# Optimization experiments

Measured on AMD Instinct MI355X. Metric: run time of the kernel, lower is better.

## Reference

```python
import jax, jax.numpy as jnp
import numpy as np

B, C, L, H, P, NF = 32, 512, 336, 1024, 192, 4  # batch, enc_in, seq_len, nflow_dim, pred_len, nflow_layers


def setup_inputs() -> dict:
    key = jax.random.key(0)
    ks = jax.random.split(key, 18)
    s = 0.02  # small init so exp(0.5*sigma) stays tame
    f32 = jnp.float32
    return {
        "x_enc": jax.random.normal(ks[0], (B, C, L), f32),
        "eps": jax.random.normal(ks[1], (B, C, P), f32),
        # GRU params (torch gate order r,z,n)
        "gru_wih": jax.random.normal(ks[2], (3 * H, C), f32) * s,
        "gru_whh": jax.random.normal(ks[3], (3 * H, H), f32) * s,
        "gru_bih": jax.random.normal(ks[4], (3 * H,), f32) * s,
        "gru_bhh": jax.random.normal(ks[5], (3 * H,), f32) * s,
        # enc_fix: Linear(1, enc_in)
        "encfix_w": jax.random.normal(ks[6], (C, 1), f32) * s,
        "encfix_b": jax.random.normal(ks[7], (C,), f32) * s,
        # distribution_enc_mu / presigma: Linear(d_ff, pred_len)
        "encmu_w": jax.random.normal(ks[8], (P, H), f32) * s,
        "encmu_b": jax.random.normal(ks[9], (P,), f32) * s,
        "encps_w": jax.random.normal(ks[10], (P, H), f32) * s,
        "encps_b": jax.random.normal(ks[11], (P,), f32) * s,
        # flow layers (stacked): Conv1d(C,C,2), Linear(H+P,P) x2
        "conv_w": jax.random.normal(ks[12], (NF, C, C, 2), f32) * s,
        "conv_b": jax.random.normal(ks[13], (NF, C), f32) * s,
        "mu_w": jax.random.normal(ks[14], (NF, P, H + P), f32) * s,
        "mu_b": jax.random.normal(ks[15], (NF, P), f32) * s,
        "sg_w": jax.random.normal(ks[16], (NF, P, H + P), f32) * s,
        "sg_b": jax.random.normal(ks[17], (NF, P), f32) * s,
    }


def reference(x_enc, eps, gru_wih, gru_whh, gru_bih, gru_bhh,
              encfix_w, encfix_b, encmu_w, encmu_b, encps_w, encps_b,
              conv_w, conv_b, mu_w, mu_b, sg_w, sg_b):
    h_dim = gru_whh.shape[1]
    pred_len = encmu_w.shape[0]
    x = jnp.transpose(x_enc, (0, 2, 1))            # (B, L, C)
    xw = x @ gru_wih.T + gru_bih                   # (B, L, 3H) input projections, precomputed

    def step(h, g):
        gh = h @ gru_whh.T + gru_bhh
        ir, iz, in_ = jnp.split(g, 3, axis=-1)
        hr, hz, hn = jnp.split(gh, 3, axis=-1)
        r = jax.nn.sigmoid(ir + hr)
        z = jax.nn.sigmoid(iz + hz)
        n = jnp.tanh(in_ + r * hn)
        return (1.0 - z) * n + z * h, None

    h0 = jnp.zeros((x.shape[0], h_dim), x.dtype)
    hT, _ = jax.lax.scan(step, h0, jnp.swapaxes(xw, 0, 1))  # (B, H) final hidden

    # enc_fix: Linear(1, enc_in) applied on last axis of (B, H, 1)
    enc = hT[:, :, None] * encfix_w[:, 0] + encfix_b        # (B, H, C)
    enc = jnp.transpose(enc, (0, 2, 1))                      # (B, C, H)

    enc_mu = enc @ encmu_w.T + encmu_b                       # (B, C, P)
    enc_sigma = jax.nn.softplus(enc @ encps_w.T + encps_b)   # (B, C, P)
    sample = enc_mu + jnp.exp(0.5 * enc_sigma) * eps         # (B, C, P)
    h = jnp.concatenate([enc, sample], axis=2)               # (B, C, H+P)

    for l in range(conv_w.shape[0]):
        w = conv_w[l]                                        # (C, C, 2)
        # Conv1d kernel size 2, valid padding, then ReLU
        hc = (jnp.einsum('bit,oi->bot', h[:, :, :-1], w[:, :, 0])
              + jnp.einsum('bit,oi->bot', h[:, :, 1:], w[:, :, 1])
              + conv_b[l][:, None])
        hc = jax.nn.relu(hc)
        hc = jnp.concatenate([hc[:, :, :1], hc], axis=2)     # re-pad to (B, C, H+P)
        mu = hc @ mu_w[l].T + mu_b[l]                        # (B, C, P)
        sg = hc @ sg_w[l].T + sg_b[l]                        # (B, C, P)
        sample = mu + jnp.exp(0.5 * sg) * sample * 0.1
        h = h + 0.1 * jnp.concatenate([hc[:, :, :hc.shape[2] - pred_len], sample], axis=2)

    return jnp.transpose(sample, (0, 2, 1))                  # (B, P, C)
```

## Files before the change

### kernel.cpp

```cpp
#include <hip/hip_runtime.h>

using u16 = unsigned short;
using u32 = unsigned int;
using u64 = unsigned long long;
using f32x4 = __attribute__((ext_vector_type(4))) float;
using s16x8 = __attribute__((ext_vector_type(8))) short;
using u32x4 = __attribute__((ext_vector_type(4))) unsigned int;

__device__ __forceinline__ u16 f2b(float f) {
  union { float f; u32 u; } v; v.f = f;
  u32 r = v.u + 0x7fffu + ((v.u >> 16) & 1u);
  return (u16)(r >> 16);
}
__device__ __forceinline__ float b2f(u16 h) {
  union { u32 u; float f; } v; v.u = ((u32)h) << 16; return v.f;
}
__device__ __forceinline__ void gl_lds16(const u16* g, u16* l) {
  __builtin_amdgcn_global_load_lds(
      (const __attribute__((address_space(1))) void*)g,
      (__attribute__((address_space(3))) void*)l, 16, 0, 0);
}
__device__ __forceinline__ float fsigm(float x) {
  return 1.f / (1.f + __expf(-x));
}
__device__ __forceinline__ float ftanh(float x) {
  float ax = fabsf(x);
  float e2 = __expf(2.f * ax);
  float th = 1.f - 2.f / (e2 + 1.f);
  return copysignf(th, x);
}

__global__ void k_cast(const float* __restrict__ s, u16* __restrict__ d, int n) {
  int i = blockIdx.x * 256 + threadIdx.x;
  if (i < n) d[i] = f2b(s[i]);
}

__global__ void k_musgw(const float* __restrict__ muw, const float* __restrict__ sgw,
                        u16* __restrict__ dst, int n) {
  int i = blockIdx.x * 256 + threadIdx.x;
  if (i >= n) return;
  int l = i / (384 * 1216);
  int r = (i / 1216) % 384;
  int k = i % 1216;
  int p = r >> 1;
  const float* s = (r & 1) ? (sgw + ((long)l * 192 + p) * 1216 + k)
                           : (muw + ((long)l * 192 + p) * 1216 + k);
  dst[i] = f2b(*s);
}

__global__ void k_catb(const float* __restrict__ mub, const float* __restrict__ sgb,
                       float* __restrict__ catb) {
  int i = blockIdx.x * 256 + threadIdx.x;
  if (i >= 1536) return;
  int l = i / 384, r = i % 384;
  int p = r >> 1;
  catb[i] = (r & 1) ? sgb[l * 192 + p] : mub[l * 192 + p];
}

__global__ void k_convw(const float* __restrict__ cw, u16* __restrict__ Aw, int n) {
  int i = blockIdx.x * 256 + threadIdx.x;
  if (i >= n) return;
  int l = i >> 19;
  int r1 = i & 524287;
  int o = r1 >> 10;
  int r2 = r1 & 1023;
  int tap = r2 >> 9;
  int ii = r2 & 511;
  Aw[i] = f2b(cw[(((long)(l * 512 + o)) * 512 + ii) * 2 + tap]);
}

__global__ void k_gruw(const float* __restrict__ whh, u16* __restrict__ blob) {
  int i = blockIdx.x * 256 + threadIdx.x;
  int lane = i & 63;
  int c = (i >> 6) & 15;
  int g = (i >> 10) % 3;
  int wwv = i / 3072;
  int wv = wwv & 3, wg = wwv >> 2;
  int jbw = wv & 1, kw = wv >> 1;
  int j = wg * 32 + jbw * 16 + (lane & 15);
  int k = kw * 512 + c * 32 + (lane >> 4) * 8;
  const float* src = whh + ((long)(g * 1024 + j)) * 1024 + k;
  u16* dst = blob + (long)i * 8;
#pragma unroll
  for (int v = 0; v < 8; ++v) dst[v] = f2b(src[v]);
}

__global__ __launch_bounds__(256) void k_txe(const float* __restrict__ x, u16* __restrict__ xT) {
  __shared__ float tile[32][33];
  int l0 = blockIdx.x * 32, c0 = blockIdx.y * 32, b = blockIdx.z;
  int tid = threadIdx.x;
  for (int q = 0; q < 4; ++q) {
    int idx = tid + q * 256;
    int r = idx >> 5, cc = idx & 31;
    int l = l0 + cc;
    tile[r][cc] = (l < 336) ? x[((long)b * 512 + c0 + r) * 336 + l] : 0.f;
  }
  __syncthreads();
  for (int q = 0; q < 4; ++q) {
    int idx = tid + q * 256;
    int r = idx >> 5, cc = idx & 31;
    int l = l0 + r;
    if (l < 336) xT[((long)b * 336 + l) * 512 + c0 + cc] = f2b(tile[cc][r]);
  }
}

__global__ __launch_bounds__(256) void k_hbt(const float* __restrict__ hbuf, u16* __restrict__ hbT) {
  __shared__ float tile[32][65];
  int t0 = blockIdx.x * 64, c0 = blockIdx.y * 32, b = blockIdx.z;
  int tid = threadIdx.x;
#pragma unroll
  for (int q = 0; q < 2; ++q) {
    int idx = tid + q * 256;
    int r = idx >> 4, col = (idx & 15) * 4;
    *(float4*)&tile[r][col] =
        *(const float4*)&hbuf[((long)b * 512 + c0 + r) * 1216 + t0 + col];
  }
  __syncthreads();
#pragma unroll
  for (int q = 0; q < 2; ++q) {
    int idx = tid + q * 256;
    int t = idx >> 3, cg = (idx & 7) * 4;
    ushort4 o;
    o.x = f2b(tile[cg + 0][t]);
    o.y = f2b(tile[cg + 1][t]);
    o.z = f2b(tile[cg + 2][t]);
    o.w = f2b(tile[cg + 3][t]);
    *(ushort4*)&hbT[((long)b * 1216 + t0 + t) * 512 + c0 + cg] = o;
  }
}

__global__ __launch_bounds__(256) void k_out(const float* __restrict__ smp, float* __restrict__ out) {
  __shared__ float tile[32][33];
  int p0 = blockIdx.x * 32, c0 = blockIdx.y * 32, b = blockIdx.z;
  int tid = threadIdx.x;
  for (int q = 0; q < 4; ++q) {
    int idx = tid + q * 256;
    int r = idx >> 5, cc = idx & 31;
    tile[r][cc] = smp[((long)b * 512 + c0 + r) * 192 + p0 + cc];
  }
  __syncthreads();
  for (int q = 0; q < 4; ++q) {
    int idx = tid + q * 256;
    int r = idx >> 5, cc = idx & 31;
    out[((long)b * 192 + p0 + r) * 512 + c0 + cc] = tile[cc][r];
  }
}

template<int MODE>
__global__ __launch_bounds__(256, 2)
void gemm_bt(const u16* __restrict__ A, const u16* __restrict__ Bt,
             void* __restrict__ Cv, const float* __restrict__ bias,
             int M, int N, int K, int lda, int ldb, int ldc,
             long sA, long sB, long sC,
             int arowmax, int browmax, int NT,
             float* __restrict__ hbufp, long sH,
             float* __restrict__ sampleP, long sS)
{
  __shared__ u16 As[128 * 64];
  __shared__ u16 Bs[128 * 64];
  const int tid = threadIdx.x;
  const int lane = tid & 63;
  const int wv = tid >> 6;
  const int z = blockIdx.z;
  const u16* Ab = A + (long)z * sA;
  const u16* Bb = Bt + (long)z * sB;
  const int m0 = blockIdx.y * 128, n0 = blockIdx.x * 128;
  const int wm = (wv >> 1) * 64, wn = (wv & 1) * 64;

  f32x4 acc[4][4] = {};

  for (int kt = 0; kt < K; kt += 64) {
#pragma unroll
    for (int s = 0; s < 4; ++s) {
      int row = (wv * 4 + s) * 8 + (lane >> 3);
      int ck = (lane & 7) ^ (row & 7);
      int ra = m0 + row; if (ra > arowmax) ra = arowmax;
      gl_lds16(Ab + (long)ra * lda + (kt + ck * 8), As + (wv * 4 + s) * 512);
      int rb = n0 + row; if (rb > browmax) rb = browmax;
      gl_lds16(Bb + (long)rb * ldb + (kt + ck * 8), Bs + (wv * 4 + s) * 512);
    }
    __syncthreads();
#pragma unroll
    for (int kk = 0; kk < 64; kk += 32) {
      s16x8 af[4], bfr[4];
#pragma unroll
      for (int i = 0; i < 4; ++i) {
        int rowa = wm + i * 16 + (lane & 15);
        int offa = (rowa * 128 + (kk + 8 * (lane >> 4)) * 2) ^ ((rowa & 7) << 4);
        af[i] = *(const s16x8*)((const char*)As + offa);
        int rowb = wn + i * 16 + (lane & 15);
        int offb = (rowb * 128 + (kk + 8 * (lane >> 4)) * 2) ^ ((rowb & 7) << 4);
        bfr[i] = *(const s16x8*)((const char*)Bs + offb);
      }
#pragma unroll
      for (int i = 0; i < 4; ++i)
#pragma unroll
        for (int j = 0; j < 4; ++j)
          acc[i][j] = __builtin_amdgcn_mfma_f32_16x16x32_bf16(af[i], bfr[j], acc[i][j], 0, 0, 0);
    }
    __syncthreads();
  }

  u16* Cb16 = (u16*)Cv;
#pragma unroll
  for (int i = 0; i < 4; ++i) {
#pragma unroll
    for (int j = 0; j < 4; ++j) {
      const int mb = m0 + wm + i * 16 + 4 * (lane >> 4);
      const int n = n0 + wn + j * 16 + (lane & 15);
      if (n >= NT) continue;
      f32x4 v = acc[i][j];
      if (MODE == 0) {
        float bn = bias[n];
        u16* Cp = Cb16;
#pragma unroll
        for (int r = 0; r < 4; ++r)
          Cp[(long)(mb + r) * ldc + n] = f2b(v[r] + bn);
      } else if (MODE == 4) {
        float bn = bias[n];
        u16* Cp = Cb16;
#pragma unroll
        for (int r = 0; r < 4; ++r) {
          int m = mb + r;
          int bb = m / 336;
          int tt = m - bb * 336;
          Cp[(long)(tt * 32 + bb) * ldc + n] = f2b(v[r] + bn);
        }
      } else if (MODE == 2) {
        u16* Cp = Cb16 + (long)z * sC;
        float* hb = hbufp + (long)z * sH;
#pragma unroll
        for (int r = 0; r < 4; ++r) {
          int m = mb + r;
          float x = v[r] + bias[m];
          x = fmaxf(x, 0.0f);
          u16 hx = f2b(x);
          Cp[(long)m * ldc + (n + 1)] = hx;
          if (n + 1 < 1024) hb[(long)m * 1216 + (n + 1)] += 0.1f * x;
          if (n == 0) { Cp[(long)m * ldc] = hx; hb[(long)m * 1216] += 0.1f * x; }
        }
      } else {
        float bn = bias[n];
        float* hb = hbufp + (long)z * sH;
        float* smp = sampleP + (long)z * sS;
        const int p = n >> 1;
#pragma unroll
        for (int r = 0; r < 4; ++r) {
          float val = v[r] + bn;
          float other = __shfl_xor(val, 1);
          if ((lane & 1) == 0) {
            int m = mb + r;
            long si = (long)m * 192 + p;
            float snew = val + __expf(0.5f * other) * smp[si] * 0.1f;
            smp[si] = snew;
            hb[(long)m * 1216 + 1024 + p] += 0.1f * snew;
          }
        }
      }
    }
  }
}

__global__ __launch_bounds__(256, 1)
void k_gru(const u16* __restrict__ xw, const u16* __restrict__ wblob,
           const float* __restrict__ bhh, u64* __restrict__ hfA, u64* __restrict__ hfB,
           float* __restrict__ hTt, float* __restrict__ hTn, u32* __restrict__ flags)
{
  __shared__ float part[6][32][32];
  const int tid = threadIdx.x;
  const int lane = tid & 63;
  const int wv = tid >> 6;
  const int wg = blockIdx.x;
  const int jbw = wv & 1, kw = wv >> 1;

  s16x8 bfr[3][16];
  {
    const u16* wp = wblob + (long)(wg * 4 + wv) * 24576 + lane * 8;
#pragma unroll
    for (int g = 0; g < 3; ++g)
#pragma unroll
      for (int c = 0; c < 16; ++c)
        bfr[g][c] = *(const s16x8*)(wp + (g * 16 + c) * 512);
  }

  const int bq = tid & 31, jg = tid >> 5;
  const int j0 = wg * 32 + jg * 4;
  float b3[3][4];
#pragma unroll
  for (int g = 0; g < 3; ++g)
#pragma unroll
    for (int jj = 0; jj < 4; ++jj) b3[g][jj] = bhh[g * 1024 + j0 + jj];
  ushort4 hold = make_ushort4(0, 0, 0, 0);

  const long hoff64 = ((long)(wg * 2 + (bq >> 4)) * 64 + (bq & 15) + 16 * (jg >> 1)) * 2 + (jg & 1);
  const int myflag = wg * 32;

  for (int t = 0; t < 336; ++t) {
    const u64* __restrict__ hr = (t & 1) ? hfB : hfA;
    u64* __restrict__ hw = (t & 1) ? hfA : hfB;

    const u16* xp = xw + ((long)t * 32 + bq) * 3072 + j0;
    ushort4 xr = *(const ushort4*)(xp);
    ushort4 xz = *(const ushort4*)(xp + 1024);
    ushort4 xn = *(const ushort4*)(xp + 2048);

    if (t > 0) {
      if (wv == 0) {
        const int fi = (lane & 31) * 32;
        int spins = 0;
        while (true) {
          u32 v = __hip_atomic_load(&flags[fi], __ATOMIC_RELAXED, __HIP_MEMORY_SCOPE_AGENT);
          if (__ballot(v >= (u32)t) == ~0ull) break;
          __builtin_amdgcn_s_sleep(1);
          if (++spins > (1 << 22)) break;
        }
      }
    }
    __syncthreads();
    __builtin_amdgcn_sched_barrier(0);

    u32x4 md[32];
#pragma unroll
    for (int c = 0; c < 16; ++c) {
      const int cg = kw * 16 + c;
      u64 a0 = (u64)(const void*)(hr + ((long)(cg * 2 + 0) * 64 + lane) * 2);
      u64 a1 = (u64)(const void*)(hr + ((long)(cg * 2 + 1) * 64 + lane) * 2);
      asm volatile("global_load_dwordx4 %0, %1, off sc1" : "=v"(md[2 * c]) : "v"(a0) : "memory");
      asm volatile("global_load_dwordx4 %0, %1, off sc1" : "=v"(md[2 * c + 1]) : "v"(a1) : "memory");
    }
    asm volatile("s_waitcnt vmcnt(0)" ::: "memory");
    __builtin_amdgcn_sched_barrier(0);

    f32x4 acc[2][3] = {};
#pragma unroll
    for (int c = 0; c < 16; ++c) {
      union { u32x4 d; s16x8 v; } a0u, a1u;
      a0u.d = md[2 * c]; a1u.d = md[2 * c + 1];
#pragma unroll
      for (int g = 0; g < 3; ++g) {
        acc[0][g] = __builtin_amdgcn_mfma_f32_16x16x32_bf16(a0u.v, bfr[g][c], acc[0][g], 0, 0, 0);
        acc[1][g] = __builtin_amdgcn_mfma_f32_16x16x32_bf16(a1u.v, bfr[g][c], acc[1][g], 0, 0, 0);
      }
    }
    {
      const int jl = jbw * 16 + (lane & 15);
      const int swz = ((jl & 1) << 4) | ((jl & 6) << 1);
      const int s4 = (lane >> 4) * 4;
#pragma unroll
      for (int p = 0; p < 2; ++p)
#pragma unroll
        for (int g = 0; g < 3; ++g)
          *(f32x4*)&part[kw * 3 + g][jl][(16 * p + s4) ^ swz] = acc[p][g];
    }
    __syncthreads();

    float hnew[4];
#pragma unroll
    for (int jj = 0; jj < 4; ++jj) {
      const int jl = jg * 4 + jj;
      const int swz = ((jl & 1) << 4) | ((jl & 6) << 1);
      const int slot = bq ^ swz;
      float s0 = part[0][jl][slot] + part[3][jl][slot] + b3[0][jj];
      float s1 = part[1][jl][slot] + part[4][jl][slot] + b3[1][jj];
      float s2 = part[2][jl][slot] + part[5][jl][slot] + b3[2][jj];
      float xrv = b2f(((const u16*)&xr)[jj]);
      float xzv = b2f(((const u16*)&xz)[jj]);
      float xnv = b2f(((const u16*)&xn)[jj]);
      float rg = fsigm(xrv + s0);
      float zg = fsigm(xzv + s1);
      float ng = ftanh(xnv + rg * s2);
      float holdv = b2f(((const u16*)&hold)[jj]);
      hnew[jj] = (1.f - zg) * ng + zg * holdv;
    }
    ((u16*)&hold)[0] = f2b(hnew[0]);
    ((u16*)&hold)[1] = f2b(hnew[1]);
    ((u16*)&hold)[2] = f2b(hnew[2]);
    ((u16*)&hold)[3] = f2b(hnew[3]);

    {
      union { ushort4 s; u32 d[2]; } hq; hq.s = hold;
      u32 p0 = (u32)__shfl_xor((int)hq.d[0], 32);
      u32 p1 = (u32)__shfl_xor((int)hq.d[1], 32);
      if ((lane & 32) == 0) {
        union { u32 d[4]; u32x4 v; } st;
        st.d[0] = hq.d[0]; st.d[1] = hq.d[1]; st.d[2] = p0; st.d[3] = p1;
        u64 ad = (u64)(void*)(hw + hoff64);
        asm volatile("global_store_dwordx4 %0, %1, off sc1" :: "v"(ad), "v"(st.v) : "memory");
      }
    }
    if (t == 335) {
#pragma unroll
      for (int jj = 0; jj < 4; ++jj) hTt[(j0 + jj) * 32 + bq] = hnew[jj];
      *(float4*)(hTn + bq * 1024 + j0) = make_float4(hnew[0], hnew[1], hnew[2], hnew[3]);
    }
    asm volatile("s_waitcnt vmcnt(0)" ::: "memory");
    __syncthreads();
    if (tid == 0)
      __hip_atomic_store(&flags[myflag], (u32)(t + 1), __ATOMIC_RELAXED, __HIP_MEMORY_SCOPE_AGENT);
  }
}

__global__ __launch_bounds__(256) void k_encsmall(
    const float* __restrict__ hTt, const float* __restrict__ emw, const float* __restrict__ epw,
    float* __restrict__ Am, float* __restrict__ Asg, float* __restrict__ Sm, float* __restrict__ Ssg)
{
  int q = blockIdx.x * 256 + threadIdx.x;
  int p = q >> 3, bg = q & 7;
  float am[4] = {0.f, 0.f, 0.f, 0.f}, as[4] = {0.f, 0.f, 0.f, 0.f};
  float sm = 0.f, ss = 0.f;
  const float* wmp = emw + (long)p * 1024;
  const float* wsp = epw + (long)p * 1024;
  for (int k = 0; k < 1024; ++k) {
    float a = wmp[k], b = wsp[k];
    f32x4 hv = *(const f32x4*)(hTt + k * 32 + bg * 4);
#pragma unroll
    for (int i = 0; i < 4; ++i) { am[i] += a * hv[i]; as[i] += b * hv[i]; }
    sm += a; ss += b;
  }
#pragma unroll
  for (int i = 0; i < 4; ++i) {
    Am[(bg * 4 + i) * 192 + p] = am[i];
    Asg[(bg * 4 + i) * 192 + p] = as[i];
  }
  if (bg == 0) { Sm[p] = sm; Ssg[p] = ss; }
}

__global__ __launch_bounds__(256) void k_build(
    const float* __restrict__ hTn, const float* __restrict__ fw, const float* __restrict__ fb,
    const float* __restrict__ Am, const float* __restrict__ Asg,
    const float* __restrict__ Sm, const float* __restrict__ Ssg,
    const float* __restrict__ emub, const float* __restrict__ epsb,
    const float* __restrict__ eps, float* __restrict__ hbuf, float* __restrict__ sample)
{
  int c = blockIdx.x, b = blockIdx.y, tid = threadIdx.x;
  float fwc = fw[c], fbc = fb[c];
  long hb0 = ((long)b * 512 + c) * 1216;
  const float* hrow = hTn + b * 1024;
  for (int q = 0; q < 4; ++q) {
    int tt = tid + q * 256;
    hbuf[hb0 + tt] = hrow[tt] * fwc + fbc;
  }
  if (tid < 192) {
    int p = tid;
    float mu_e = fwc * Am[b * 192 + p] + fbc * Sm[p] + emub[p];
    float pse = fwc * Asg[b * 192 + p] + fbc * Ssg[p] + epsb[p];
    float sgv = (pse > 15.f) ? pse : log1pf(__expf(pse));
    long si = ((long)b * 512 + c) * 192 + p;
    float smp = mu_e + __expf(0.5f * sgv) * eps[si];
    sample[si] = smp;
    hbuf[hb0 + 1024 + p] = smp;
  }
}

extern "C" void kernel_launch(void* const* d_in, const int* in_sizes, int n_in,
                              void* d_out, int out_size, void* d_ws, size_t ws_size,
                              hipStream_t stream)
{
  const float* x_enc = (const float*)d_in[0];
  const float* eps   = (const float*)d_in[1];
  const float* wih   = (const float*)d_in[2];
  const float* whh   = (const float*)d_in[3];
  const float* bih   = (const float*)d_in[4];
  const float* bhh   = (const float*)d_in[5];
  const float* fw    = (const float*)d_in[6];
  const float* fb    = (const float*)d_in[7];
  const float* emw   = (const float*)d_in[8];
  const float* emub  = (const float*)d_in[9];
  const float* epw   = (const float*)d_in[10];
  const float* epsb  = (const float*)d_in[11];
  const float* cw    = (const float*)d_in[12];
  const float* cb    = (const float*)d_in[13];
  const float* muw   = (const float*)d_in[14];
  const float* mub   = (const float*)d_in[15];
  const float* sgw   = (const float*)d_in[16];
  const float* sgwb  = (const float*)d_in[17];
  float* out = (float*)d_out;

  char* w = (char*)d_ws;
  auto alloc = [&](size_t bytes) { char* p = w; w += (bytes + 255) & ~(size_t)255; return p; };
  u16* Aw       = (u16*)alloc(4ull * 512 * 1024 * 2);
  u16* musgw16  = (u16*)alloc(4ull * 384 * 1216 * 2);
  u16* wih16    = (u16*)alloc(3072ull * 512 * 2);
  u64* hfA      = (u64*)alloc(65536);
  u64* hfB      = (u64*)alloc(65536);
  u32* flags    = (u32*)alloc(4096);
  float* catb   = (float*)alloc(1536 * 4);
  float* hTt    = (float*)alloc(131072);
  float* hTn    = (float*)alloc(131072);
  float* Am     = (float*)alloc(32 * 192 * 4);
  float* Asg    = (float*)alloc(32 * 192 * 4);
  float* Sm     = (float*)alloc(1024);
  float* Ssg    = (float*)alloc(1024);
  float* smp    = (float*)alloc(32ull * 512 * 192 * 4);
  u16* hcB      = (u16*)alloc(32ull * 512 * 1216 * 2);
  char* un1     = alloc(32ull * 512 * 1216 * 4);
  u16* xw       = (u16*)un1;
  float* hbuf   = (float*)un1;
  char* un2     = alloc(32ull * 1216 * 512 * 2);
  u16* xT       = (u16*)un2;
  u16* hbT      = (u16*)un2;
  u16* wblob    = hcB;

  if ((size_t)(w - (char*)d_ws) > ws_size) return;

  hipMemsetAsync(hfA, 0, 65536, stream);
  hipMemsetAsync(hfB, 0, 65536, stream);
  hipMemsetAsync(flags, 0, 4096, stream);

  k_cast<<<dim3((3072 * 512 + 255) / 256), 256, 0, stream>>>(wih, wih16, 3072 * 512);
  k_musgw<<<dim3((4 * 384 * 1216 + 255) / 256), 256, 0, stream>>>(muw, sgw, musgw16, 4 * 384 * 1216);
  k_catb<<<dim3(6), 256, 0, stream>>>(mub, sgwb, catb);
  k_convw<<<dim3((4 * 512 * 1024 + 255) / 256), 256, 0, stream>>>(cw, Aw, 4 * 512 * 1024);
  k_gruw<<<dim3(1536), 256, 0, stream>>>(whh, wblob);
  k_txe<<<dim3(11, 16, 32), 256, 0, stream>>>(x_enc, xT);

  gemm_bt<4><<<dim3(24, 84, 1), 256, 0, stream>>>(xT, wih16, xw, bih,
      10752, 3072, 512, 512, 512, 3072, 0, 0, 0, 10751, 3071, 3072,
      nullptr, 0, nullptr, 0);

  k_gru<<<dim3(32), 256, 0, stream>>>(xw, wblob, bhh, hfA, hfB, hTt, hTn, flags);

  k_encsmall<<<dim3(6), 256, 0, stream>>>(hTt, emw, epw, Am, Asg, Sm, Ssg);
  k_build<<<dim3(512, 32), 256, 0, stream>>>(hTn, fw, fb, Am, Asg, Sm, Ssg, emub, epsb, eps, hbuf, smp);

  for (int l = 0; l < 4; ++l) {
    k_hbt<<<dim3(19, 16, 32), 256, 0, stream>>>(hbuf, hbT);
    gemm_bt<2><<<dim3(10, 4, 32), 256, 0, stream>>>(Aw + (long)l * 512 * 1024, hbT, hcB, cb + l * 512,
        512, 1215, 1024, 1024, 512, 1216, 0, 1216 * 512, 512 * 1216, 511, 1214, 1215,
        hbuf, 512 * 1216, nullptr, 0);
    gemm_bt<5><<<dim3(3, 4, 32), 256, 0, stream>>>(hcB, musgw16 + (long)l * 384 * 1216, nullptr, catb + l * 384,
        512, 384, 1216, 1216, 1216, 384, 512 * 1216, 0, 0, 511, 383, 384,
        hbuf, 512 * 1216, smp, 512 * 192);
  }

  k_out<<<dim3(6, 16, 32), 256, 0, stream>>>(smp, out);
}
```

Baseline: 2.373 ms.

## Split GRU recurrence across two independent batch halves with 64 workgroups

The persistent GRU kernel now launches 64 workgroups instead of 32. Each batch half of 16 rows gets its own group of 32 workgroups with a separate flag array, so the two halves synchronize independently. Each workgroup does half the MFMA work and half the hidden-state loads per timestep, which shortens the per-step critical path of the serial recurrence. In exchange, the whole Whh is replicated in registers across twice as many CUs, and half of the threads sit idle during the gate computation.

```diff
diff --git a/kernel.cpp b/kernel.cpp
--- a/kernel.cpp
+++ b/kernel.cpp
@@ -270,12 +270,14 @@
   const int tid = threadIdx.x;
   const int lane = tid & 63;
   const int wv = tid >> 6;
-  const int wg = blockIdx.x;
+  const int q = (int)(blockIdx.x >> 5);
+  const int tw = (int)(blockIdx.x & 31);
   const int jbw = wv & 1, kw = wv >> 1;
+  u32* __restrict__ myflags = flags + q * 1024;
 
   s16x8 bfr[3][16];
   {
-    const u16* wp = wblob + (long)(wg * 4 + wv) * 24576 + lane * 8;
+    const u16* wp = wblob + (long)(tw * 4 + wv) * 24576 + lane * 8;
 #pragma unroll
     for (int g = 0; g < 3; ++g)
 #pragma unroll
@@ -283,8 +285,9 @@
         bfr[g][c] = *(const s16x8*)(wp + (g * 16 + c) * 512);
   }
 
-  const int bq = tid & 31, jg = tid >> 5;
-  const int j0 = wg * 32 + jg * 4;
+  const int bq16 = tid & 15, jg = (tid >> 4) & 7;
+  const int j0 = tw * 32 + jg * 4;
+  const int bb = q * 16 + bq16;
   float b3[3][4];
 #pragma unroll
   for (int g = 0; g < 3; ++g)
@@ -292,24 +295,27 @@
     for (int jj = 0; jj < 4; ++jj) b3[g][jj] = bhh[g * 1024 + j0 + jj];
   ushort4 hold = make_ushort4(0, 0, 0, 0);
 
-  const long hoff64 = ((long)(wg * 2 + (bq >> 4)) * 64 + (bq & 15) + 16 * (jg >> 1)) * 2 + (jg & 1);
-  const int myflag = wg * 32;
+  const long hoff64 = (long)(tw * 2 + q) * 128 + ((long)(jg >> 1) * 16 + bq16) * 2;
+  const int myflag = tw * 32;
 
   for (int t = 0; t < 336; ++t) {
     const u64* __restrict__ hr = (t & 1) ? hfB : hfA;
     u64* __restrict__ hw = (t & 1) ? hfA : hfB;
 
-    const u16* xp = xw + ((long)t * 32 + bq) * 3072 + j0;
-    ushort4 xr = *(const ushort4*)(xp);
-    ushort4 xz = *(const ushort4*)(xp + 1024);
-    ushort4 xn = *(const ushort4*)(xp + 2048);
+    ushort4 xr = {}, xz = {}, xn = {};
+    if (tid < 128) {
+      const u16* xp = xw + ((long)t * 32 + bb) * 3072 + j0;
+      xr = *(const ushort4*)(xp);
+      xz = *(const ushort4*)(xp + 1024);
+      xn = *(const ushort4*)(xp + 2048);
+    }
 
     if (t > 0) {
       if (wv == 0) {
         const int fi = (lane & 31) * 32;
         int spins = 0;
         while (true) {
-          u32 v = __hip_atomic_load(&flags[fi], __ATOMIC_RELAXED, __HIP_MEMORY_SCOPE_AGENT);
+          u32 v = __hip_atomic_load(&myflags[fi], __ATOMIC_RELAXED, __HIP_MEMORY_SCOPE_AGENT);
           if (__ballot(v >= (u32)t) == ~0ull) break;
           __builtin_amdgcn_s_sleep(1);
           if (++spins > (1 << 22)) break;
@@ -319,84 +325,80 @@
     __syncthreads();
     __builtin_amdgcn_sched_barrier(0);
 
-    u32x4 md[32];
+    u32x4 md[16];
 #pragma unroll
     for (int c = 0; c < 16; ++c) {
       const int cg = kw * 16 + c;
-      u64 a0 = (u64)(const void*)(hr + ((long)(cg * 2 + 0) * 64 + lane) * 2);
-      u64 a1 = (u64)(const void*)(hr + ((long)(cg * 2 + 1) * 64 + lane) * 2);
-      asm volatile("global_load_dwordx4 %0, %1, off sc1" : "=v"(md[2 * c]) : "v"(a0) : "memory");
-      asm volatile("global_load_dwordx4 %0, %1, off sc1" : "=v"(md[2 * c + 1]) : "v"(a1) : "memory");
+      u64 a0 = (u64)(const void*)(hr + ((long)(cg * 2 + q) * 64 + lane) * 2);
+      asm volatile("global_load_dwordx4 %0, %1, off sc1" : "=v"(md[c]) : "v"(a0) : "memory");
     }
     asm volatile("s_waitcnt vmcnt(0)" ::: "memory");
     __builtin_amdgcn_sched_barrier(0);
 
-    f32x4 acc[2][3] = {};
+    f32x4 acc[3] = {};
 #pragma unroll
     for (int c = 0; c < 16; ++c) {
-      union { u32x4 d; s16x8 v; } a0u, a1u;
-      a0u.d = md[2 * c]; a1u.d = md[2 * c + 1];
-#pragma unroll
-      for (int g = 0; g < 3; ++g) {
-        acc[0][g] = __builtin_amdgcn_mfma_f32_16x16x32_bf16(a0u.v, bfr[g][c], acc[0][g], 0, 0, 0);
-        acc[1][g] = __builtin_amdgcn_mfma_f32_16x16x32_bf16(a1u.v, bfr[g][c], acc[1][g], 0, 0, 0);
-      }
+      union { u32x4 d; s16x8 v; } au;
+      au.d = md[c];
+#pragma unroll
+      for (int g = 0; g < 3; ++g)
+        acc[g] = __builtin_amdgcn_mfma_f32_16x16x32_bf16(au.v, bfr[g][c], acc[g], 0, 0, 0);
     }
     {
       const int jl = jbw * 16 + (lane & 15);
       const int swz = ((jl & 1) << 4) | ((jl & 6) << 1);
       const int s4 = (lane >> 4) * 4;
 #pragma unroll
-      for (int p = 0; p < 2; ++p)
-#pragma unroll
-        for (int g = 0; g < 3; ++g)
-          *(f32x4*)&part[kw * 3 + g][jl][(16 * p + s4) ^ swz] = acc[p][g];
+      for (int g = 0; g < 3; ++g)
+        *(f32x4*)&part[kw * 3 + g][jl][(16 * q + s4) ^ swz] = acc[g];
     }
     __syncthreads();
 
-    float hnew[4];
-#pragma unroll
-    for (int jj = 0; jj < 4; ++jj) {
-      const int jl = jg * 4 + jj;
-      const int swz = ((jl & 1) << 4) | ((jl & 6) << 1);
-      const int slot = bq ^ swz;
-      float s0 = part[0][jl][slot] + part[3][jl][slot] + b3[0][jj];
-      float s1 = part[1][jl][slot] + part[4][jl][slot] + b3[1][jj];
-      float s2 = part[2][jl][slot] + part[5][jl][slot] + b3[2][jj];
-      float xrv = b2f(((const u16*)&xr)[jj]);
-      float xzv = b2f(((const u16*)&xz)[jj]);
-      float xnv = b2f(((const u16*)&xn)[jj]);
-      float rg = fsigm(xrv + s0);
-      float zg = fsigm(xzv + s1);
-      float ng = ftanh(xnv + rg * s2);
-      float holdv = b2f(((const u16*)&hold)[jj]);
-      hnew[jj] = (1.f - zg) * ng + zg * holdv;
-    }
-    ((u16*)&hold)[0] = f2b(hnew[0]);
-    ((u16*)&hold)[1] = f2b(hnew[1]);
-    ((u16*)&hold)[2] = f2b(hnew[2]);
-    ((u16*)&hold)[3] = f2b(hnew[3]);
-
-    {
-      union { ushort4 s; u32 d[2]; } hq; hq.s = hold;
-      u32 p0 = (u32)__shfl_xor((int)hq.d[0], 32);
-      u32 p1 = (u32)__shfl_xor((int)hq.d[1], 32);
-      if ((lane & 32) == 0) {
-        union { u32 d[4]; u32x4 v; } st;
-        st.d[0] = hq.d[0]; st.d[1] = hq.d[1]; st.d[2] = p0; st.d[3] = p1;
-        u64 ad = (u64)(void*)(hw + hoff64);
-        asm volatile("global_store_dwordx4 %0, %1, off sc1" :: "v"(ad), "v"(st.v) : "memory");
+    if (tid < 128) {
+      float hnew[4];
+#pragma unroll
+      for (int jj = 0; jj < 4; ++jj) {
+        const int jl = jg * 4 + jj;
+        const int swz = ((jl & 1) << 4) | ((jl & 6) << 1);
+        const int slot = (16 * q + bq16) ^ swz;
+        float s0 = part[0][jl][slot] + part[3][jl][slot] + b3[0][jj];
+        float s1 = part[1][jl][slot] + part[4][jl][slot] + b3[1][jj];
+        float s2 = part[2][jl][slot] + part[5][jl][slot] + b3[2][jj];
+        float xrv = b2f(((const u16*)&xr)[jj]);
+        float xzv = b2f(((const u16*)&xz)[jj]);
+        float xnv = b2f(((const u16*)&xn)[jj]);
+        float rg = fsigm(xrv + s0);
+        float zg = fsigm(xzv + s1);
+        float ng = ftanh(xnv + rg * s2);
+        float holdv = b2f(((const u16*)&hold)[jj]);
+        hnew[jj] = (1.f - zg) * ng + zg * holdv;
       }
-    }
-    if (t == 335) {
-#pragma unroll
-      for (int jj = 0; jj < 4; ++jj) hTt[(j0 + jj) * 32 + bq] = hnew[jj];
-      *(float4*)(hTn + bq * 1024 + j0) = make_float4(hnew[0], hnew[1], hnew[2], hnew[3]);
+      ((u16*)&hold)[0] = f2b(hnew[0]);
+      ((u16*)&hold)[1] = f2b(hnew[1]);
+      ((u16*)&hold)[2] = f2b(hnew[2]);
+      ((u16*)&hold)[3] = f2b(hnew[3]);
+
+      {
+        union { ushort4 s; u32 d[2]; } hq; hq.s = hold;
+        u32 p0 = (u32)__shfl_xor((int)hq.d[0], 16);
+        u32 p1 = (u32)__shfl_xor((int)hq.d[1], 16);
+        if ((lane & 16) == 0) {
+          union { u32 d[4]; u32x4 v; } st;
+          st.d[0] = hq.d[0]; st.d[1] = hq.d[1]; st.d[2] = p0; st.d[3] = p1;
+          u64 ad = (u64)(void*)(hw + hoff64);
+          asm volatile("global_store_dwordx4 %0, %1, off sc1" :: "v"(ad), "v"(st.v) : "memory");
+        }
+      }
+      if (t == 335) {
+#pragma unroll
+        for (int jj = 0; jj < 4; ++jj) hTt[(j0 + jj) * 32 + bb] = hnew[jj];
+        *(float4*)(hTn + bb * 1024 + j0) = make_float4(hnew[0], hnew[1], hnew[2], hnew[3]);
+      }
     }
     asm volatile("s_waitcnt vmcnt(0)" ::: "memory");
     __syncthreads();
     if (tid == 0)
-      __hip_atomic_store(&flags[myflag], (u32)(t + 1), __ATOMIC_RELAXED, __HIP_MEMORY_SCOPE_AGENT);
+      __hip_atomic_store(&myflags[myflag], (u32)(t + 1), __ATOMIC_RELAXED, __HIP_MEMORY_SCOPE_AGENT);
   }
 }
 
@@ -483,7 +485,7 @@
   u16* wih16    = (u16*)alloc(3072ull * 512 * 2);
   u64* hfA      = (u64*)alloc(65536);
   u64* hfB      = (u64*)alloc(65536);
-  u32* flags    = (u32*)alloc(4096);
+  u32* flags    = (u32*)alloc(8192);
   float* catb   = (float*)alloc(1536 * 4);
   float* hTt    = (float*)alloc(131072);
   float* hTn    = (float*)alloc(131072);
@@ -505,7 +507,7 @@
 
   hipMemsetAsync(hfA, 0, 65536, stream);
   hipMemsetAsync(hfB, 0, 65536, stream);
-  hipMemsetAsync(flags, 0, 4096, stream);
+  hipMemsetAsync(flags, 0, 8192, stream);
 
   k_cast<<<dim3((3072 * 512 + 255) / 256), 256, 0, stream>>>(wih, wih16, 3072 * 512);
   k_musgw<<<dim3((4 * 384 * 1216 + 255) / 256), 256, 0, stream>>>(muw, sgw, musgw16, 4 * 384 * 1216);
@@ -518,7 +520,7 @@
       10752, 3072, 512, 512, 512, 3072, 0, 0, 0, 10751, 3071, 3072,
       nullptr, 0, nullptr, 0);
 
-  k_gru<<<dim3(32), 256, 0, stream>>>(xw, wblob, bhh, hfA, hfB, hTt, hTn, flags);
+  k_gru<<<dim3(64), 256, 0, stream>>>(xw, wblob, bhh, hfA, hfB, hTt, hTn, flags);
 
   k_encsmall<<<dim3(6), 256, 0, stream>>>(hTt, emw, epw, Am, Asg, Sm, Ssg);
   k_build<<<dim3(512, 32), 256, 0, stream>>>(hTn, fw, fb, Am, Asg, Sm, Ssg, emub, epsb, eps, hbuf, smp);
```

Measured after the change: 2.121 ms. 10.6% less time.
